# Kernel optimization log

Measured on AMD Instinct MI355X. Metric: run time of the kernel, lower is better.

## Reference

```python
import jax, jax.numpy as jnp
import numpy as np

B, T, F, D, H = 16, 512, 32, 256, 256
EPS = 1e-5


def _layernorm(y, g, b):
    m = jnp.mean(y, axis=-1, keepdims=True)
    v = jnp.mean((y - m) ** 2, axis=-1, keepdims=True)
    return (y - m) / jnp.sqrt(v + EPS) * g + b


def setup_inputs() -> dict:
    key = jax.random.key(0)
    ks = jax.random.split(key, 24)
    s = lambda fan_in: 1.0 / np.sqrt(fan_in)
    u = lambda k, shape, fan_in: jax.random.uniform(k, shape, jnp.float32, -s(fan_in), s(fan_in))
    return {
        "x": jax.random.normal(ks[0], (B, T, F), jnp.float32),
        # per-feature Linear(1, D), stacked over F
        "proj_w": u(ks[1], (F, D), 1),
        "proj_b": u(ks[2], (F, D), 1),
        # per-feature scorer GRN(D, H, 1), stacked over F
        "sc_fc1_w": u(ks[3], (F, H, D), D),
        "sc_fc1_b": u(ks[4], (F, H), D),
        "sc_fc2_w": u(ks[5], (F, 1, H), H),
        "sc_fc2_b": u(ks[6], (F, 1), H),
        "sc_gate_w": u(ks[7], (F, 1, 1), 1),
        "sc_gate_b": u(ks[8], (F, 1), 1),
        "sc_skip_w": u(ks[9], (F, 1, D), D),
        "sc_skip_b": u(ks[10], (F, 1), D),
        "sc_ln_g": jnp.ones((F, 1), jnp.float32),
        "sc_ln_b": jnp.zeros((F, 1), jnp.float32),
        # post GRN(D, H, D); in_dim == out_dim -> skip is identity
        "post_fc1_w": u(ks[11], (H, D), D),
        "post_fc1_b": u(ks[12], (H,), D),
        "post_fc2_w": u(ks[13], (D, H), H),
        "post_fc2_b": u(ks[14], (D,), H),
        "post_gate_w": u(ks[15], (D, D), D),
        "post_gate_b": u(ks[16], (D,), D),
        "post_ln_g": jnp.ones((D,), jnp.float32),
        "post_ln_b": jnp.zeros((D,), jnp.float32),
    }


def reference(x, proj_w, proj_b, sc_fc1_w, sc_fc1_b, sc_fc2_w, sc_fc2_b,
              sc_gate_w, sc_gate_b, sc_skip_w, sc_skip_b, sc_ln_g, sc_ln_b,
              post_fc1_w, post_fc1_b, post_fc2_w, post_fc2_b,
              post_gate_w, post_gate_b, post_ln_g, post_ln_b):
    # per-feature embedding: Linear(1 -> D), batched over F
    # E: [B, T, F, D]
    E = x[..., None] * proj_w[None, None] + proj_b[None, None]

    # per-feature scorer GRN(D, H, 1), all F at once
    h = jax.nn.elu(jnp.einsum("btfd,fhd->btfh", E, sc_fc1_w) + sc_fc1_b)
    h = jnp.einsum("btfh,foh->btfo", h, sc_fc2_w) + sc_fc2_b  # [B,T,F,1]
    g = jax.nn.sigmoid(jnp.einsum("btfo,fpo->btfp", h, sc_gate_w) + sc_gate_b)
    skip = jnp.einsum("btfd,fod->btfo", E, sc_skip_w) + sc_skip_b
    y = g * h + (1.0 - g) * skip
    S = _layernorm(y, sc_ln_g, sc_ln_b)  # [B,T,F,1] (last dim size 1)

    # softmax over features, weighted mixture
    W = jax.nn.softmax(S, axis=2)
    mix = jnp.sum(E * W, axis=2)  # [B,T,D]

    # post GRN(D, H, D), skip = identity
    h2 = jax.nn.elu(mix @ post_fc1_w.T + post_fc1_b)
    h2 = h2 @ post_fc2_w.T + post_fc2_b
    g2 = jax.nn.sigmoid(h2 @ post_gate_w.T + post_gate_b)
    y2 = g2 * h2 + (1.0 - g2) * mix
    return _layernorm(y2, post_ln_g, post_ln_b)
```

## Files before the change

kernel.cpp:

```cpp
#include <hip/hip_runtime.h>
#include <hip/hip_bf16.h>
#include <math.h>


typedef __bf16 bf16;
typedef __bf16 bf16x8 __attribute__((ext_vector_type(8)));
typedef __bf16 bf16x4 __attribute__((ext_vector_type(4)));
typedef float f32x4 __attribute__((ext_vector_type(4)));

#define NTOK 8192
#define D_   256
#define F_   32

#define OFF_C      512
#define OFF_BP     1536
#define OFF_WPROJT 4096
#define OFF_FC1    32768
#define OFF_FC2    163840
#define OFF_GF     294912


__global__ __launch_bounds__(256) void vsn_prep(
    const float* __restrict__ proj_w, const float* __restrict__ proj_b,
    const float* __restrict__ sc_ln_b,
    const float* __restrict__ fc1w, const float* __restrict__ fc2w,
    const float* __restrict__ fc2b,
    const float* __restrict__ gatew, const float* __restrict__ gateb,
    float* __restrict__ wsC, float* __restrict__ wsBp, bf16* __restrict__ wsWT,
    bf16* __restrict__ oFC1, bf16* __restrict__ oFC2, bf16* __restrict__ oGF)
{
  const int blk = blockIdx.x;
  if (blk < 16) {
    int g = blk * 256 + threadIdx.x;
    int m = g >> 11;
    int c = g & 2047;
    const float* src = (m == 0) ? fc1w : fc2w;
    bf16* dst = (m == 0) ? oFC1 : oFC2;
    int row = c >> 3, ks = c & 7;
    int j = row >> 4, lm = row & 15;
    const float* sp = src + row * 256 + ks * 32;
    bf16* dp = dst + j * 4096 + ks * 512 + lm * 32;
    #pragma unroll
    for (int q = 0; q < 4; q++) {
      float4 a = ((const float4*)sp)[2 * q];
      float4 b = ((const float4*)sp)[2 * q + 1];
      bf16x8 v = {(bf16)a.x, (bf16)a.y, (bf16)a.z, (bf16)a.w,
                  (bf16)b.x, (bf16)b.y, (bf16)b.z, (bf16)b.w};
      *(bf16x8*)(dp + q * 8) = v;
    }
  } else if (blk == 16) {
    const int d = threadIdx.x;
    float wv[F_];
    float mx = -3.0e38f;
    #pragma unroll
    for (int f = 0; f < F_; f++) { wv[f] = sc_ln_b[f]; mx = fmaxf(mx, wv[f]); }
    float se = 0.0f;
    #pragma unroll
    for (int f = 0; f < F_; f++) { wv[f] = __expf(wv[f] - mx); se += wv[f]; }
    float inv = 1.0f / se;
    float acc = 0.0f;
    #pragma unroll
    for (int f = 0; f < F_; f++) {
      float wf = wv[f] * inv;
      acc += wf * proj_b[f * D_ + d];
      wsWT[d * F_ + f] = (bf16)(wf * proj_w[f * D_ + d]);
    }
    wsC[d] = acc;
  } else {
    __shared__ float gs[4][257];
    const int rb = (blk - 17) * 4;
    const int c = threadIdx.x;
    #pragma unroll
    for (int r = 0; r < 4; r++) gs[r][c] = gatew[(rb + r) * 256 + c];
    __syncthreads();
    float a0 = 0.f, a1 = 0.f, a2 = 0.f, a3 = 0.f;
    for (int k = 0; k < 256; k++) {
      float f = fc2w[k * 256 + c];
      a0 += gs[0][k] * f;
      a1 += gs[1][k] * f;
      a2 += gs[2][k] * f;
      a3 += gs[3][k] * f;
    }
    float accr[4] = {a0, a1, a2, a3};
    #pragma unroll
    for (int r = 0; r < 4; r++) {
      int row = rb + r;
      oGF[(row >> 4) * 4096 + (c >> 5) * 512 + (row & 15) * 32 + (c & 31)] =
          (bf16)accr[r];
    }
    if (c < 4) {
      float s = gateb[rb + c];
      for (int k = 0; k < 256; k++) s += gs[c][k] * fc2b[k];
      wsBp[rb + c] = s;
    }
  }
}

__global__ __launch_bounds__(256, 1) void vsn_main(
    const float* __restrict__ x,
    const float* __restrict__ wsC,
    const bf16* __restrict__ WT,
    const bf16* __restrict__ FC1, const float* __restrict__ fc1_b,
    const bf16* __restrict__ FC2, const float* __restrict__ fc2_b,
    const bf16* __restrict__ GF, const float* __restrict__ bprime,
    const float* __restrict__ ln_g, const float* __restrict__ ln_b,
    float* __restrict__ out)
{
  __shared__ bf16  sAct[2][32][264];
  __shared__ float sLN[4][32][2];

  const int tid  = threadIdx.x;
  const int w    = tid >> 6;
  const int lane = tid & 63;
  const int lm   = lane & 15;
  const int lq   = lane >> 4;
  const int j0   = w * 4;
  const int tok0 = blockIdx.x * 32;

  bf16x4 mixh[2][4];
  {
    bf16x8 a[2];
    #pragma unroll
    for (int t = 0; t < 2; t++) {
      const float* xp = x + (size_t)(tok0 + t * 16 + lm) * F_ + lq * 8;
      float4 x0 = *(const float4*)xp;
      float4 x1 = *(const float4*)(xp + 4);
      bf16x8 av = {(bf16)x0.x, (bf16)x0.y, (bf16)x0.z, (bf16)x0.w,
                   (bf16)x1.x, (bf16)x1.y, (bf16)x1.z, (bf16)x1.w};
      a[t] = av;
    }
    #pragma unroll
    for (int jj = 0; jj < 4; jj++) {
      int n = (j0 + jj) * 16 + lm;
      bf16x8 b = *(const bf16x8*)(WT + n * F_ + lq * 8);
      float cv = wsC[n];
      #pragma unroll
      for (int t = 0; t < 2; t++) {
        f32x4 acc = {cv, cv, cv, cv};
        acc = __builtin_amdgcn_mfma_f32_16x16x32_bf16(a[t], b, acc, 0, 0, 0);
        bf16x4 mh = {(bf16)acc[0], (bf16)acc[1], (bf16)acc[2], (bf16)acc[3]};
        mixh[t][jj] = mh;
        #pragma unroll
        for (int r = 0; r < 4; r++) sAct[0][t * 16 + lq * 4 + r][n] = mh[r];
      }
    }
  }
  __syncthreads();

  {
    bf16x8 af[2][8];
    #pragma unroll
    for (int t = 0; t < 2; t++)
      #pragma unroll
      for (int ks = 0; ks < 8; ks++)
        af[t][ks] = *(const bf16x8*)(&sAct[0][t * 16 + lm][ks * 32 + lq * 8]);
    const bf16* base = FC1 + j0 * 4096 + lm * 32 + lq * 8;
    bf16x8 bb[8];
    #pragma unroll
    for (int ks = 0; ks < 8; ks++)
      bb[ks] = *(const bf16x8*)(base + ks * 512);
    #pragma unroll
    for (int jj = 0; jj < 4; jj++) {
      bf16x8 bn[8];
      if (jj < 3) {
        const bf16* nb = base + (jj + 1) * 4096;
        #pragma unroll
        for (int ks = 0; ks < 8; ks++)
          bn[ks] = *(const bf16x8*)(nb + ks * 512);
      }
      f32x4 acc0 = {0.f, 0.f, 0.f, 0.f}, acc1 = {0.f, 0.f, 0.f, 0.f};
      #pragma unroll
      for (int ks = 0; ks < 8; ks++) {
        acc0 = __builtin_amdgcn_mfma_f32_16x16x32_bf16(af[0][ks], bb[ks], acc0, 0, 0, 0);
        acc1 = __builtin_amdgcn_mfma_f32_16x16x32_bf16(af[1][ks], bb[ks], acc1, 0, 0, 0);
      }
      int n = (j0 + jj) * 16 + lm;
      float bias = fc1_b[n];
      #pragma unroll
      for (int r = 0; r < 4; r++) {
        float v0 = acc0[r] + bias;
        v0 = (v0 > 0.0f) ? v0 : (__expf(v0) - 1.0f);
        sAct[1][lq * 4 + r][n] = (bf16)v0;
        float v1 = acc1[r] + bias;
        v1 = (v1 > 0.0f) ? v1 : (__expf(v1) - 1.0f);
        sAct[1][16 + lq * 4 + r][n] = (bf16)v1;
      }
      if (jj < 3) {
        #pragma unroll
        for (int ks = 0; ks < 8; ks++) bb[ks] = bn[ks];
      }
    }
  }
  __syncthreads();

  f32x4 y2[2][4];
  {
    bf16x8 af[2][8];
    #pragma unroll
    for (int t = 0; t < 2; t++)
      #pragma unroll
      for (int ks = 0; ks < 8; ks++)
        af[t][ks] = *(const bf16x8*)(&sAct[1][t * 16 + lm][ks * 32 + lq * 8]);
    const bf16* baseF = FC2 + j0 * 4096 + lm * 32 + lq * 8;
    const bf16* baseG = GF  + j0 * 4096 + lm * 32 + lq * 8;
    #pragma unroll
    for (int jj = 0; jj < 4; jj++) {
      bf16x8 bF[8], bG[8];
      #pragma unroll
      for (int ks = 0; ks < 8; ks++) {
        bF[ks] = *(const bf16x8*)(baseF + jj * 4096 + ks * 512);
        bG[ks] = *(const bf16x8*)(baseG + jj * 4096 + ks * 512);
      }
      f32x4 hF0 = {0.f,0.f,0.f,0.f}, hF1 = {0.f,0.f,0.f,0.f};
      f32x4 hG0 = {0.f,0.f,0.f,0.f}, hG1 = {0.f,0.f,0.f,0.f};
      #pragma unroll
      for (int ks = 0; ks < 8; ks++) {
        hF0 = __builtin_amdgcn_mfma_f32_16x16x32_bf16(af[0][ks], bF[ks], hF0, 0, 0, 0);
        hF1 = __builtin_amdgcn_mfma_f32_16x16x32_bf16(af[1][ks], bF[ks], hF1, 0, 0, 0);
        hG0 = __builtin_amdgcn_mfma_f32_16x16x32_bf16(af[0][ks], bG[ks], hG0, 0, 0, 0);
        hG1 = __builtin_amdgcn_mfma_f32_16x16x32_bf16(af[1][ks], bG[ks], hG1, 0, 0, 0);
      }
      int n = (j0 + jj) * 16 + lm;
      float b2v = fc2_b[n];
      float bpv = bprime[n];
      #pragma unroll
      for (int r = 0; r < 4; r++) {
        float h20 = hF0[r] + b2v;
        float g0  = 1.0f / (1.0f + __expf(-(hG0[r] + bpv)));
        y2[0][jj][r] = g0 * h20 + (1.0f - g0) * (float)mixh[0][jj][r];
        float h21 = hF1[r] + b2v;
        float g1  = 1.0f / (1.0f + __expf(-(hG1[r] + bpv)));
        y2[1][jj][r] = g1 * h21 + (1.0f - g1) * (float)mixh[1][jj][r];
      }
    }
  }

  #pragma unroll
  for (int t = 0; t < 2; t++) {
    float rs[4] = {0.f,0.f,0.f,0.f}, rq[4] = {0.f,0.f,0.f,0.f};
    #pragma unroll
    for (int jj = 0; jj < 4; jj++)
      #pragma unroll
      for (int r = 0; r < 4; r++) {
        float y = y2[t][jj][r];
        rs[r] += y;
        rq[r] += y * y;
      }
    #pragma unroll
    for (int r = 0; r < 4; r++) {
      #pragma unroll
      for (int off = 1; off < 16; off <<= 1) {
        rs[r] += __shfl_xor(rs[r], off);
        rq[r] += __shfl_xor(rq[r], off);
      }
      if (lm == 0) {
        sLN[w][t * 16 + lq * 4 + r][0] = rs[r];
        sLN[w][t * 16 + lq * 4 + r][1] = rq[r];
      }
    }
  }
  __syncthreads();

  const float inv_d = 1.0f / 256.0f;
  #pragma unroll
  for (int t = 0; t < 2; t++) {
    float mean[4], rstd[4];
    #pragma unroll
    for (int r = 0; r < 4; r++) {
      int row = t * 16 + lq * 4 + r;
      float S = sLN[0][row][0] + sLN[1][row][0] + sLN[2][row][0] + sLN[3][row][0];
      float Q = sLN[0][row][1] + sLN[1][row][1] + sLN[2][row][1] + sLN[3][row][1];
      float m = S * inv_d;
      mean[r] = m;
      rstd[r] = rsqrtf(Q * inv_d - m * m + 1e-5f);
    }
    #pragma unroll
    for (int jj = 0; jj < 4; jj++) {
      int n = (j0 + jj) * 16 + lm;
      float lg = ln_g[n], lb = ln_b[n];
      #pragma unroll
      for (int r = 0; r < 4; r++) {
        float o = (y2[t][jj][r] - mean[r]) * rstd[r] * lg + lb;
        out[(size_t)(tok0 + t * 16 + lq * 4 + r) * D_ + n] = o;
      }
    }
  }
}

extern "C" void kernel_launch(void* const* d_in, const int* in_sizes, int n_in,
                              void* d_out, int out_size, void* d_ws, size_t ws_size,
                              hipStream_t stream) {
  (void)in_sizes; (void)n_in; (void)ws_size; (void)out_size;
  const float* x      = (const float*)d_in[0];
  const float* proj_w = (const float*)d_in[1];
  const float* proj_b = (const float*)d_in[2];
  const float* sclnb  = (const float*)d_in[12];
  const float* fc1w   = (const float*)d_in[13];
  const float* fc1b   = (const float*)d_in[14];
  const float* fc2w   = (const float*)d_in[15];
  const float* fc2b   = (const float*)d_in[16];
  const float* gw     = (const float*)d_in[17];
  const float* gb     = (const float*)d_in[18];
  const float* lng    = (const float*)d_in[19];
  const float* lnb    = (const float*)d_in[20];

  char* ws = (char*)d_ws;
  float* wsC   = (float*)(ws + OFF_C);
  float* wsBp  = (float*)(ws + OFF_BP);
  bf16*  wsWT  = (bf16*)(ws + OFF_WPROJT);
  bf16*  bFC1  = (bf16*)(ws + OFF_FC1);
  bf16*  bFC2  = (bf16*)(ws + OFF_FC2);
  bf16*  bGF   = (bf16*)(ws + OFF_GF);

  vsn_prep<<<81, 256, 0, stream>>>(proj_w, proj_b, sclnb, fc1w, fc2w, fc2b,
                                   gw, gb, wsC, wsBp, wsWT, bFC1, bFC2, bGF);
  vsn_main<<<NTOK / 32, 256, 0, stream>>>(x, wsC, wsWT,
                                          bFC1, fc1b, bFC2, fc2b, bGF, wsBp,
                                          lng, lnb, (float*)d_out);
}
```

Before: 130.4 us.

## Use MFMA for gate-fc2 weight fusion in prep and software-pipeline main kernel weight loads

```diff
diff --git a/kernel.cpp b/kernel.cpp
--- a/kernel.cpp
+++ b/kernel.cpp
@@ -30,16 +30,17 @@
     bf16* __restrict__ oFC1, bf16* __restrict__ oFC2, bf16* __restrict__ oGF)
 {
   const int blk = blockIdx.x;
+  const int tid = threadIdx.x;
   if (blk < 16) {
-    int g = blk * 256 + threadIdx.x;
+    int g = blk * 256 + tid;
     int m = g >> 11;
     int c = g & 2047;
     const float* src = (m == 0) ? fc1w : fc2w;
     bf16* dst = (m == 0) ? oFC1 : oFC2;
     int row = c >> 3, ks = c & 7;
-    int j = row >> 4, lm = row & 15;
+    int j = row >> 4, lmr = row & 15;
     const float* sp = src + row * 256 + ks * 32;
-    bf16* dp = dst + j * 4096 + ks * 512 + lm * 32;
+    bf16* dp = dst + j * 4096 + ks * 512 + lmr * 32;
     #pragma unroll
     for (int q = 0; q < 4; q++) {
       float4 a = ((const float4*)sp)[2 * q];
@@ -49,7 +50,7 @@
       *(bf16x8*)(dp + q * 8) = v;
     }
   } else if (blk == 16) {
-    const int d = threadIdx.x;
+    const int d = tid;
     float wv[F_];
     float mx = -3.0e38f;
     #pragma unroll
@@ -66,33 +67,51 @@
       wsWT[d * F_ + f] = (bf16)(wf * proj_w[f * D_ + d]);
     }
     wsC[d] = acc;
+  } else if (blk < 81) {
+    const int w    = tid >> 6;
+    const int lane = tid & 63;
+    const int lm   = lane & 15;
+    const int lq   = lane >> 4;
+    const int id   = (blk - 17) * 4 + w;
+    const int tm   = id >> 4, tn = id & 15;
+    f32x4 acc = {0.f, 0.f, 0.f, 0.f};
+    #pragma unroll
+    for (int kb = 0; kb < 8; kb++) {
+      const float* ap = gatew + (size_t)(tm * 16 + lm) * 256 + kb * 32 + lq * 8;
+      float4 a0 = *(const float4*)ap;
+      float4 a1 = *(const float4*)(ap + 4);
+      bf16x8 av = {(bf16)a0.x, (bf16)a0.y, (bf16)a0.z, (bf16)a0.w,
+                   (bf16)a1.x, (bf16)a1.y, (bf16)a1.z, (bf16)a1.w};
+      bf16x8 bv;
+      #pragma unroll
+      for (int j = 0; j < 8; j++)
+        bv[j] = (bf16)fc2w[(size_t)(kb * 32 + lq * 8 + j) * 256 + tn * 16 + lm];
+      acc = __builtin_amdgcn_mfma_f32_16x16x32_bf16(av, bv, acc, 0, 0, 0);
+    }
+    bf16* dp = oGF + tm * 4096 + (tn >> 1) * 512 + (tn & 1) * 16 + lm;
+    #pragma unroll
+    for (int r = 0; r < 4; r++)
+      dp[(lq * 4 + r) * 32] = (bf16)acc[r];
   } else {
-    __shared__ float gs[4][257];
-    const int rb = (blk - 17) * 4;
-    const int c = threadIdx.x;
-    #pragma unroll
-    for (int r = 0; r < 4; r++) gs[r][c] = gatew[(rb + r) * 256 + c];
+    __shared__ float sB[256];
+    __shared__ float sRed[64][4];
+    sB[tid] = fc2b[tid];
     __syncthreads();
-    float a0 = 0.f, a1 = 0.f, a2 = 0.f, a3 = 0.f;
-    for (int k = 0; k < 256; k++) {
-      float f = fc2w[k * 256 + c];
-      a0 += gs[0][k] * f;
-      a1 += gs[1][k] * f;
-      a2 += gs[2][k] * f;
-      a3 += gs[3][k] * f;
-    }
-    float accr[4] = {a0, a1, a2, a3};
-    #pragma unroll
-    for (int r = 0; r < 4; r++) {
-      int row = rb + r;
-      oGF[(row >> 4) * 4096 + (c >> 5) * 512 + (row & 15) * 32 + (c & 31)] =
-          (bf16)accr[r];
-    }
-    if (c < 4) {
-      float s = gateb[rb + c];
-      for (int k = 0; k < 256; k++) s += gs[c][k] * fc2b[k];
-      wsBp[rb + c] = s;
-    }
+    const int row = (blk - 81) * 64 + (tid >> 2);
+    const int ch  = tid & 3;
+    const float4* gp = (const float4*)(gatew + (size_t)row * 256 + ch * 64);
+    float p = 0.0f;
+    #pragma unroll
+    for (int q = 0; q < 16; q++) {
+      float4 g = gp[q];
+      int e = ch * 64 + q * 4;
+      p += g.x * sB[e] + g.y * sB[e + 1] + g.z * sB[e + 2] + g.w * sB[e + 3];
+    }
+    sRed[tid >> 2][ch] = p;
+    __syncthreads();
+    if (ch == 0)
+      wsBp[row] = gateb[row] + sRed[tid >> 2][0] + sRed[tid >> 2][1] +
+                  sRed[tid >> 2][2] + sRed[tid >> 2][3];
   }
 }
 
@@ -117,123 +136,148 @@
   const int j0   = w * 4;
   const int tok0 = blockIdx.x * 32;
 
-  bf16x4 mixh[2][4];
-  {
-    bf16x8 a[2];
+  int nn[4];
+  float cv[4], b1v[4], b2v[4], bpv[4], lgv[4], lbv[4];
+  #pragma unroll
+  for (int jj = 0; jj < 4; jj++) {
+    nn[jj]  = (j0 + jj) * 16 + lm;
+    cv[jj]  = wsC[nn[jj]];
+    b1v[jj] = fc1_b[nn[jj]];
+    b2v[jj] = fc2_b[nn[jj]];
+    bpv[jj] = bprime[nn[jj]];
+    lgv[jj] = ln_g[nn[jj]];
+    lbv[jj] = ln_b[nn[jj]];
+  }
+  bf16x8 aX[2];
+  #pragma unroll
+  for (int t = 0; t < 2; t++) {
+    const float* xp = x + (size_t)(tok0 + t * 16 + lm) * F_ + lq * 8;
+    float4 x0 = *(const float4*)xp;
+    float4 x1 = *(const float4*)(xp + 4);
+    bf16x8 av = {(bf16)x0.x, (bf16)x0.y, (bf16)x0.z, (bf16)x0.w,
+                 (bf16)x1.x, (bf16)x1.y, (bf16)x1.z, (bf16)x1.w};
+    aX[t] = av;
+  }
+  bf16x8 bWT[4];
+  #pragma unroll
+  for (int jj = 0; jj < 4; jj++)
+    bWT[jj] = *(const bf16x8*)(WT + nn[jj] * F_ + lq * 8);
+
+  const bf16* f1base = FC1 + j0 * 4096 + lm * 32 + lq * 8;
+  bf16x8 b0[8], b1[8], b2[8], b3[8];
+  #pragma unroll
+  for (int ks = 0; ks < 8; ks++)
+    b0[ks] = *(const bf16x8*)(f1base + ks * 512);
+
+  f32x4 mixf[2][4];
+  #pragma unroll
+  for (int jj = 0; jj < 4; jj++) {
     #pragma unroll
     for (int t = 0; t < 2; t++) {
-      const float* xp = x + (size_t)(tok0 + t * 16 + lm) * F_ + lq * 8;
-      float4 x0 = *(const float4*)xp;
-      float4 x1 = *(const float4*)(xp + 4);
-      bf16x8 av = {(bf16)x0.x, (bf16)x0.y, (bf16)x0.z, (bf16)x0.w,
-                   (bf16)x1.x, (bf16)x1.y, (bf16)x1.z, (bf16)x1.w};
-      a[t] = av;
-    }
-    #pragma unroll
-    for (int jj = 0; jj < 4; jj++) {
-      int n = (j0 + jj) * 16 + lm;
-      bf16x8 b = *(const bf16x8*)(WT + n * F_ + lq * 8);
-      float cv = wsC[n];
-      #pragma unroll
-      for (int t = 0; t < 2; t++) {
-        f32x4 acc = {cv, cv, cv, cv};
-        acc = __builtin_amdgcn_mfma_f32_16x16x32_bf16(a[t], b, acc, 0, 0, 0);
-        bf16x4 mh = {(bf16)acc[0], (bf16)acc[1], (bf16)acc[2], (bf16)acc[3]};
-        mixh[t][jj] = mh;
-        #pragma unroll
-        for (int r = 0; r < 4; r++) sAct[0][t * 16 + lq * 4 + r][n] = mh[r];
-      }
+      f32x4 acc = {cv[jj], cv[jj], cv[jj], cv[jj]};
+      acc = __builtin_amdgcn_mfma_f32_16x16x32_bf16(aX[t], bWT[jj], acc, 0, 0, 0);
+      mixf[t][jj] = acc;
+      bf16x4 mh = {(bf16)acc[0], (bf16)acc[1], (bf16)acc[2], (bf16)acc[3]};
+      #pragma unroll
+      for (int r = 0; r < 4; r++) sAct[0][t * 16 + lq * 4 + r][nn[jj]] = mh[r];
     }
   }
   __syncthreads();
 
-  {
-    bf16x8 af[2][8];
-    #pragma unroll
-    for (int t = 0; t < 2; t++)
-      #pragma unroll
-      for (int ks = 0; ks < 8; ks++)
-        af[t][ks] = *(const bf16x8*)(&sAct[0][t * 16 + lm][ks * 32 + lq * 8]);
-    const bf16* base = FC1 + j0 * 4096 + lm * 32 + lq * 8;
-    bf16x8 bb[8];
+  bf16x8 af[2][8];
+  #pragma unroll
+  for (int t = 0; t < 2; t++)
     #pragma unroll
     for (int ks = 0; ks < 8; ks++)
-      bb[ks] = *(const bf16x8*)(base + ks * 512);
-    #pragma unroll
-    for (int jj = 0; jj < 4; jj++) {
-      bf16x8 bn[8];
-      if (jj < 3) {
-        const bf16* nb = base + (jj + 1) * 4096;
-        #pragma unroll
-        for (int ks = 0; ks < 8; ks++)
-          bn[ks] = *(const bf16x8*)(nb + ks * 512);
-      }
-      f32x4 acc0 = {0.f, 0.f, 0.f, 0.f}, acc1 = {0.f, 0.f, 0.f, 0.f};
-      #pragma unroll
-      for (int ks = 0; ks < 8; ks++) {
-        acc0 = __builtin_amdgcn_mfma_f32_16x16x32_bf16(af[0][ks], bb[ks], acc0, 0, 0, 0);
-        acc1 = __builtin_amdgcn_mfma_f32_16x16x32_bf16(af[1][ks], bb[ks], acc1, 0, 0, 0);
-      }
-      int n = (j0 + jj) * 16 + lm;
-      float bias = fc1_b[n];
-      #pragma unroll
-      for (int r = 0; r < 4; r++) {
-        float v0 = acc0[r] + bias;
-        v0 = (v0 > 0.0f) ? v0 : (__expf(v0) - 1.0f);
-        sAct[1][lq * 4 + r][n] = (bf16)v0;
-        float v1 = acc1[r] + bias;
-        v1 = (v1 > 0.0f) ? v1 : (__expf(v1) - 1.0f);
-        sAct[1][16 + lq * 4 + r][n] = (bf16)v1;
-      }
-      if (jj < 3) {
-        #pragma unroll
-        for (int ks = 0; ks < 8; ks++) bb[ks] = bn[ks];
-      }
-    }
-  }
+      af[t][ks] = *(const bf16x8*)(&sAct[0][t * 16 + lm][ks * 32 + lq * 8]);
+
+  const bf16* f2base = FC2 + j0 * 4096 + lm * 32 + lq * 8;
+  const bf16* gfbase = GF  + j0 * 4096 + lm * 32 + lq * 8;
+  bf16x8 cF[8], cG[8];
+
+  auto ph2_mfma = [&](const bf16x8* bb, int jj) {
+    f32x4 a0 = {0.f, 0.f, 0.f, 0.f}, a1 = {0.f, 0.f, 0.f, 0.f};
+    #pragma unroll
+    for (int ks = 0; ks < 8; ks++) {
+      a0 = __builtin_amdgcn_mfma_f32_16x16x32_bf16(af[0][ks], bb[ks], a0, 0, 0, 0);
+      a1 = __builtin_amdgcn_mfma_f32_16x16x32_bf16(af[1][ks], bb[ks], a1, 0, 0, 0);
+    }
+    #pragma unroll
+    for (int r = 0; r < 4; r++) {
+      float v0 = a0[r] + b1v[jj];
+      v0 = (v0 > 0.0f) ? v0 : (__expf(v0) - 1.0f);
+      sAct[1][lq * 4 + r][nn[jj]] = (bf16)v0;
+      float v1 = a1[r] + b1v[jj];
+      v1 = (v1 > 0.0f) ? v1 : (__expf(v1) - 1.0f);
+      sAct[1][16 + lq * 4 + r][nn[jj]] = (bf16)v1;
+    }
+  };
+
+  #pragma unroll
+  for (int ks = 0; ks < 8; ks++) b1[ks] = *(const bf16x8*)(f1base + 4096 + ks * 512);
+  ph2_mfma(b0, 0);
+  #pragma unroll
+  for (int ks = 0; ks < 8; ks++) b2[ks] = *(const bf16x8*)(f1base + 8192 + ks * 512);
+  ph2_mfma(b1, 1);
+  #pragma unroll
+  for (int ks = 0; ks < 8; ks++) b3[ks] = *(const bf16x8*)(f1base + 12288 + ks * 512);
+  #pragma unroll
+  for (int ks = 0; ks < 8; ks++) {
+    cF[ks] = *(const bf16x8*)(f2base + ks * 512);
+    cG[ks] = *(const bf16x8*)(gfbase + ks * 512);
+  }
+  ph2_mfma(b2, 2);
+  ph2_mfma(b3, 3);
   __syncthreads();
 
+  #pragma unroll
+  for (int t = 0; t < 2; t++)
+    #pragma unroll
+    for (int ks = 0; ks < 8; ks++)
+      af[t][ks] = *(const bf16x8*)(&sAct[1][t * 16 + lm][ks * 32 + lq * 8]);
+
   f32x4 y2[2][4];
-  {
-    bf16x8 af[2][8];
-    #pragma unroll
-    for (int t = 0; t < 2; t++)
-      #pragma unroll
-      for (int ks = 0; ks < 8; ks++)
-        af[t][ks] = *(const bf16x8*)(&sAct[1][t * 16 + lm][ks * 32 + lq * 8]);
-    const bf16* baseF = FC2 + j0 * 4096 + lm * 32 + lq * 8;
-    const bf16* baseG = GF  + j0 * 4096 + lm * 32 + lq * 8;
-    #pragma unroll
-    for (int jj = 0; jj < 4; jj++) {
-      bf16x8 bF[8], bG[8];
-      #pragma unroll
-      for (int ks = 0; ks < 8; ks++) {
-        bF[ks] = *(const bf16x8*)(baseF + jj * 4096 + ks * 512);
-        bG[ks] = *(const bf16x8*)(baseG + jj * 4096 + ks * 512);
-      }
-      f32x4 hF0 = {0.f,0.f,0.f,0.f}, hF1 = {0.f,0.f,0.f,0.f};
-      f32x4 hG0 = {0.f,0.f,0.f,0.f}, hG1 = {0.f,0.f,0.f,0.f};
-      #pragma unroll
-      for (int ks = 0; ks < 8; ks++) {
-        hF0 = __builtin_amdgcn_mfma_f32_16x16x32_bf16(af[0][ks], bF[ks], hF0, 0, 0, 0);
-        hF1 = __builtin_amdgcn_mfma_f32_16x16x32_bf16(af[1][ks], bF[ks], hF1, 0, 0, 0);
-        hG0 = __builtin_amdgcn_mfma_f32_16x16x32_bf16(af[0][ks], bG[ks], hG0, 0, 0, 0);
-        hG1 = __builtin_amdgcn_mfma_f32_16x16x32_bf16(af[1][ks], bG[ks], hG1, 0, 0, 0);
-      }
-      int n = (j0 + jj) * 16 + lm;
-      float b2v = fc2_b[n];
-      float bpv = bprime[n];
-      #pragma unroll
-      for (int r = 0; r < 4; r++) {
-        float h20 = hF0[r] + b2v;
-        float g0  = 1.0f / (1.0f + __expf(-(hG0[r] + bpv)));
-        y2[0][jj][r] = g0 * h20 + (1.0f - g0) * (float)mixh[0][jj][r];
-        float h21 = hF1[r] + b2v;
-        float g1  = 1.0f / (1.0f + __expf(-(hG1[r] + bpv)));
-        y2[1][jj][r] = g1 * h21 + (1.0f - g1) * (float)mixh[1][jj][r];
-      }
-    }
-  }
+  bf16x8 dF[8], dG[8];
+  auto ph3_step = [&](const bf16x8* bF, const bf16x8* bG, int jj) {
+    f32x4 hF0 = {0.f,0.f,0.f,0.f}, hF1 = {0.f,0.f,0.f,0.f};
+    f32x4 hG0 = {0.f,0.f,0.f,0.f}, hG1 = {0.f,0.f,0.f,0.f};
+    #pragma unroll
+    for (int ks = 0; ks < 8; ks++) {
+      hF0 = __builtin_amdgcn_mfma_f32_16x16x32_bf16(af[0][ks], bF[ks], hF0, 0, 0, 0);
+      hF1 = __builtin_amdgcn_mfma_f32_16x16x32_bf16(af[1][ks], bF[ks], hF1, 0, 0, 0);
+      hG0 = __builtin_amdgcn_mfma_f32_16x16x32_bf16(af[0][ks], bG[ks], hG0, 0, 0, 0);
+      hG1 = __builtin_amdgcn_mfma_f32_16x16x32_bf16(af[1][ks], bG[ks], hG1, 0, 0, 0);
+    }
+    #pragma unroll
+    for (int r = 0; r < 4; r++) {
+      float h20 = hF0[r] + b2v[jj];
+      float g0  = 1.0f / (1.0f + __expf(-(hG0[r] + bpv[jj])));
+      y2[0][jj][r] = g0 * h20 + (1.0f - g0) * mixf[0][jj][r];
+      float h21 = hF1[r] + b2v[jj];
+      float g1  = 1.0f / (1.0f + __expf(-(hG1[r] + bpv[jj])));
+      y2[1][jj][r] = g1 * h21 + (1.0f - g1) * mixf[1][jj][r];
+    }
+  };
+
+  #pragma unroll
+  for (int ks = 0; ks < 8; ks++) {
+    dF[ks] = *(const bf16x8*)(f2base + 4096 + ks * 512);
+    dG[ks] = *(const bf16x8*)(gfbase + 4096 + ks * 512);
+  }
+  ph3_step(cF, cG, 0);
+  #pragma unroll
+  for (int ks = 0; ks < 8; ks++) {
+    cF[ks] = *(const bf16x8*)(f2base + 8192 + ks * 512);
+    cG[ks] = *(const bf16x8*)(gfbase + 8192 + ks * 512);
+  }
+  ph3_step(dF, dG, 1);
+  #pragma unroll
+  for (int ks = 0; ks < 8; ks++) {
+    dF[ks] = *(const bf16x8*)(f2base + 12288 + ks * 512);
+    dG[ks] = *(const bf16x8*)(gfbase + 12288 + ks * 512);
+  }
+  ph3_step(cF, cG, 2);
+  ph3_step(dF, dG, 3);
 
   #pragma unroll
   for (int t = 0; t < 2; t++) {
@@ -276,12 +320,10 @@
     }
     #pragma unroll
     for (int jj = 0; jj < 4; jj++) {
-      int n = (j0 + jj) * 16 + lm;
-      float lg = ln_g[n], lb = ln_b[n];
       #pragma unroll
       for (int r = 0; r < 4; r++) {
-        float o = (y2[t][jj][r] - mean[r]) * rstd[r] * lg + lb;
-        out[(size_t)(tok0 + t * 16 + lq * 4 + r) * D_ + n] = o;
+        float o = (y2[t][jj][r] - mean[r]) * rstd[r] * lgv[jj] + lbv[jj];
+        out[(size_t)(tok0 + t * 16 + lq * 4 + r) * D_ + nn[jj]] = o;
       }
     }
   }
@@ -305,14 +347,14 @@
   const float* lnb    = (const float*)d_in[20];
 
   char* ws = (char*)d_ws;
-  float* wsC   = (float*)(ws + OFF_C);
-  float* wsBp  = (float*)(ws + OFF_BP);
-  bf16*  wsWT  = (bf16*)(ws + OFF_WPROJT);
-  bf16*  bFC1  = (bf16*)(ws + OFF_FC1);
-  bf16*  bFC2  = (bf16*)(ws + OFF_FC2);
-  bf16*  bGF   = (bf16*)(ws + OFF_GF);
-
-  vsn_prep<<<81, 256, 0, stream>>>(proj_w, proj_b, sclnb, fc1w, fc2w, fc2b,
+  float* wsC  = (float*)(ws + OFF_C);
+  float* wsBp = (float*)(ws + OFF_BP);
+  bf16*  wsWT = (bf16*)(ws + OFF_WPROJT);
+  bf16*  bFC1 = (bf16*)(ws + OFF_FC1);
+  bf16*  bFC2 = (bf16*)(ws + OFF_FC2);
+  bf16*  bGF  = (bf16*)(ws + OFF_GF);
+
+  vsn_prep<<<85, 256, 0, stream>>>(proj_w, proj_b, sclnb, fc1w, fc2w, fc2b,
                                    gw, gb, wsC, wsBp, wsWT, bFC1, bFC2, bGF);
   vsn_main<<<NTOK / 32, 256, 0, stream>>>(x, wsC, wsWT,
                                           bFC1, fc1b, bFC2, fc2b, bGF, wsBp,
```

Result: faster. 119.4 us (-8.4%).
